# Kernel optimization log

Hardware: AMD Instinct MI355X
Metric: run time of the kernel (lower is better)

Reference implementation:

```python
import jax, jax.numpy as jnp
import numpy as np

D_MODEL = 1024
NUM_HEADS = 16
DEPTH = D_MODEL // NUM_HEADS
BATCH = 2
SEQ = 2048


def setup_inputs() -> dict:
    key = jax.random.key(0)
    ks = jax.random.split(key, 12)
    s = 1.0 / np.sqrt(D_MODEL)
    inp = {
        "v": jax.random.normal(ks[0], (BATCH, SEQ, D_MODEL), jnp.float32),
        "k": jax.random.normal(ks[1], (BATCH, SEQ, D_MODEL), jnp.float32),
        "q": jax.random.normal(ks[2], (BATCH, SEQ, D_MODEL), jnp.float32),
        # padding mask: 1 = masked, 0 = attend; float, broadcastable to (B,H,Sq,Sk)
        "mask": jax.random.randint(ks[3], (BATCH, 1, 1, SEQ), 0, 2).astype(jnp.float32),
        "training": 0,
        "wq_w": jax.random.normal(ks[4], (D_MODEL, D_MODEL), jnp.float32) * s,
        "wq_b": jnp.zeros((D_MODEL,), jnp.float32),
        "wk_w": jax.random.normal(ks[5], (D_MODEL, D_MODEL), jnp.float32) * s,
        "wk_b": jnp.zeros((D_MODEL,), jnp.float32),
        "wv_w": jax.random.normal(ks[6], (D_MODEL, D_MODEL), jnp.float32) * s,
        "wv_b": jnp.zeros((D_MODEL,), jnp.float32),
        "wo_w": jax.random.normal(ks[7], (D_MODEL, D_MODEL), jnp.float32) * s,
        "wo_b": jnp.zeros((D_MODEL,), jnp.float32),
    }
    return inp


def _split_heads(x, b):
    # (B, S, D) -> (B, H, S, depth)
    return x.reshape(b, -1, NUM_HEADS, DEPTH).transpose(0, 2, 1, 3)


def reference(v, k, q, mask, training, wq_w, wq_b, wk_w, wk_b, wv_w, wv_b, wo_w, wo_b):
    b = q.shape[0]
    qp = q @ wq_w + wq_b
    kp = k @ wk_w + wk_b
    vp = v @ wv_w + wv_b
    qh = _split_heads(qp, b)  # (B,H,Sq,depth)
    kh = _split_heads(kp, b)
    vh = _split_heads(vp, b)

    scale = 1.0 / jnp.sqrt(jnp.asarray(DEPTH, jnp.float32))
    logits = jnp.einsum("bhqd,bhkd->bhqk", qh, kh) * scale
    logits = logits + mask * (-1e9)
    attn = jax.nn.softmax(logits, axis=-1)                 # used for the value matmul
    out_h = jnp.einsum("bhqk,bhkd->bhqd", attn, vh)
    # NOTE: the original returns a second softmax over axis=2 (query axis)
    attn_weights = jax.nn.softmax(logits, axis=2)

    concat = out_h.transpose(0, 2, 1, 3).reshape(b, -1, D_MODEL)
    output = concat @ wo_w + wo_b
    return output, attn_weights
```

## Files before the change

kernel.cpp:

```cpp
#include <hip/hip_runtime.h>


typedef unsigned short u16;
typedef __attribute__((ext_vector_type(8))) short short8;
typedef __attribute__((ext_vector_type(8))) _Float16 half8;
typedef __attribute__((ext_vector_type(4))) float f32x4;

#define SEQ 2048
#define DMODEL 1024
#define NHEAD 16
#define DH 64

__device__ __forceinline__ u16 f2h(float f) {
  _Float16 h = (_Float16)f;
  return __builtin_bit_cast(u16, h);
}

__device__ __forceinline__ void gload16(const void* g, void* l) {
  __builtin_amdgcn_global_load_lds(
      (__attribute__((address_space(1))) void*)const_cast<void*>(g),
      (__attribute__((address_space(3))) void*)l, 16, 0, 0);
}

__global__ __launch_bounds__(256) void conv_qkv_k(
    const float* __restrict__ qs, const float* __restrict__ ks,
    const float* __restrict__ vs, u16* __restrict__ xq,
    u16* __restrict__ xk, u16* __restrict__ xv)
{
  int z = blockIdx.y;
  const float* s = (z == 0) ? qs : ((z == 1) ? ks : vs);
  u16* d = (z == 0) ? xq : ((z == 1) ? xk : xv);
  size_t i = ((size_t)blockIdx.x * 256 + threadIdx.x) * 8;
  float4 a = *(const float4*)(s + i);
  float4 b = *(const float4*)(s + i + 4);
  short8 o;
  o[0] = (short)f2h(a.x); o[1] = (short)f2h(a.y);
  o[2] = (short)f2h(a.z); o[3] = (short)f2h(a.w);
  o[4] = (short)f2h(b.x); o[5] = (short)f2h(b.y);
  o[6] = (short)f2h(b.z); o[7] = (short)f2h(b.w);
  *(short8*)(d + i) = o;
}

__global__ __launch_bounds__(256) void conv_wt_k(
    const float* __restrict__ w0, const float* __restrict__ w1,
    const float* __restrict__ w2, const float* __restrict__ w3,
    u16* __restrict__ t0, u16* __restrict__ t1,
    u16* __restrict__ t2, u16* __restrict__ t3)
{
  __shared__ u16 tile[64][65];
  int z = blockIdx.z;
  const float* W = (z==0)?w0:((z==1)?w1:((z==2)?w2:w3));
  u16* T = (z==0)?t0:((z==1)?t1:((z==2)?t2:t3));
  int k0 = blockIdx.x*64, n0 = blockIdx.y*64;
  int t = threadIdx.x;
  #pragma unroll
  for (int i=0;i<4;i++) {
    int idx = t + i*256;
    int r = idx >> 4, c4 = (idx & 15)*4;
    float4 f = *(const float4*)(W + (size_t)(k0+r)*DMODEL + n0 + c4);
    tile[r][c4+0] = f2h(f.x); tile[r][c4+1] = f2h(f.y);
    tile[r][c4+2] = f2h(f.z); tile[r][c4+3] = f2h(f.w);
  }
  __syncthreads();
  #pragma unroll
  for (int i=0;i<2;i++) {
    int idx = t + i*256;
    int nr = idx >> 3, c8 = (idx & 7)*8;
    short8 o;
    #pragma unroll
    for (int j=0;j<8;j++) o[j] = (short)tile[c8+j][nr];
    *(short8*)(T + (size_t)(n0+nr)*DMODEL + k0 + c8) = o;
  }
}

template<int EPI>
__global__ __launch_bounds__(256) void gemm16_k(
    const u16* __restrict__ A, const u16* __restrict__ Bt,
    const float* __restrict__ bias, void* __restrict__ outp)
{
  __shared__ u16 As[128*64];
  __shared__ u16 Bs[64*64];
  const int K = 1024;
  int tid = threadIdx.x, w = tid>>6, l = tid&63;
  int m0 = blockIdx.x*128, n0 = blockIdx.y*64;
  int wm = (w>>1)*64, wn = (w&1)*32;
  const f32x4 z4 = {0.f,0.f,0.f,0.f};
  f32x4 acc[4][2];
  #pragma unroll
  for (int mf=0;mf<4;mf++)
    #pragma unroll
    for (int nf=0;nf<2;nf++) acc[mf][nf] = z4;

  for (int k0=0;k0<K;k0+=64) {
    #pragma unroll
    for (int i=0;i<4;i++) {
      int cd = (w*4+i)*64 + l, r = cd>>3, p = cd&7, c = p ^ (r&7);
      gload16(A + (size_t)(m0+r)*K + k0 + c*8, (char*)As + (w*4+i)*1024);
    }
    #pragma unroll
    for (int i=0;i<2;i++) {
      int cd = (w*2+i)*64 + l, r = cd>>3, p = cd&7, c = p ^ (r&7);
      gload16(Bt + (size_t)(n0+r)*K + k0 + c*8, (char*)Bs + (w*2+i)*1024);
    }
    __syncthreads();
    half8 a[4][2], b[2][2];
    #pragma unroll
    for (int mf=0;mf<4;mf++)
      #pragma unroll
      for (int kf=0;kf<2;kf++) {
        int row = wm + mf*16 + (l&15);
        int ch = (kf*4 + (l>>4)) ^ (row&7);
        a[mf][kf] = *(const half8*)&As[row*64 + ch*8];
      }
    #pragma unroll
    for (int nf=0;nf<2;nf++)
      #pragma unroll
      for (int kf=0;kf<2;kf++) {
        int row = wn + nf*16 + (l&15);
        int ch = (kf*4 + (l>>4)) ^ (row&7);
        b[nf][kf] = *(const half8*)&Bs[row*64 + ch*8];
      }
    #pragma unroll
    for (int kf=0;kf<2;kf++)
      #pragma unroll
      for (int mf=0;mf<4;mf++)
        #pragma unroll
        for (int nf=0;nf<2;nf++)
          acc[mf][nf] = __builtin_amdgcn_mfma_f32_16x16x32_f16(
              a[mf][kf], b[nf][kf], acc[mf][nf], 0,0,0);
    __syncthreads();
  }
  #pragma unroll
  for (int mf=0;mf<4;mf++)
    #pragma unroll
    for (int nf=0;nf<2;nf++)
      #pragma unroll
      for (int r=0;r<4;r++) {
        int m = m0 + wm + mf*16 + (l>>4)*4 + r;
        int n = n0 + wn + nf*16 + (l&15);
        float v = acc[mf][nf][r] + bias[n];
        if (EPI == 0) {
          int bb = m >> 11, s = m & 2047, hh = n >> 6, dd = n & 63;
          ((u16*)outp)[((size_t)((bb*16+hh)*2048 + s))*64 + dd] = f2h(v);
        } else if (EPI == 1) {
          int bb = m >> 11, s = m & 2047, hh = n >> 6, dd = n & 63;
          ((u16*)outp)[((size_t)((bb*16+hh)*64 + dd))*2048 + s] = f2h(v);
        } else {
          ((float*)outp)[(size_t)m*DMODEL + n] = v;
        }
      }
}

__global__ __launch_bounds__(256) void flash_k(
    const u16* __restrict__ Qh, const u16* __restrict__ Kh,
    const u16* __restrict__ Vt, const float* __restrict__ mask,
    u16* __restrict__ Cc, float* __restrict__ colsum)
{
  __shared__ u16 Ks[2][64*64];
  __shared__ u16 Vs[2][64*64];
  __shared__ u16 Ps[4][16*64];
  __shared__ float colbuf[SEQ];
  int tid = threadIdx.x, w = tid>>6, l = tid&63;
  int lg = l>>4, li = l&15;
  int qb = blockIdx.x, bh = blockIdx.y, b = bh>>4, h = bh&15;
  const u16* Qb = Qh + (size_t)bh*SEQ*DH;
  const u16* Kb = Kh + (size_t)bh*SEQ*DH;
  const u16* Vb = Vt + (size_t)bh*DH*SEQ;
  const float* mrow = mask + (size_t)b*SEQ;
  for (int i=tid;i<SEQ;i+=256) colbuf[i] = 0.f;
  int q0 = qb*64 + w*16;
  half8 qf[2];
  #pragma unroll
  for (int kf=0;kf<2;kf++)
    qf[kf] = *(const half8*)&Qb[(size_t)(q0+li)*DH + kf*32 + lg*8];
  const f32x4 z4 = {0.f,0.f,0.f,0.f};
  f32x4 acc[4];
  float lrow[4];
  #pragma unroll
  for (int df=0;df<4;df++) acc[df] = z4;
  #pragma unroll
  for (int r=0;r<4;r++) lrow[r] = 0.f;
  u16* Pw = &Ps[w][0];

  auto stage = [&](int buf, int kt) {
    int k0 = kt*64;
    #pragma unroll
    for (int i=0;i<2;i++) {
      int cd = (w*2+i)*64 + l, r = cd>>3, p = cd&7, c = p ^ (r&7);
      gload16(Kb + (size_t)(k0+r)*DH + c*8, (char*)&Ks[buf][0] + (w*2+i)*1024);
    }
    #pragma unroll
    for (int i=0;i<2;i++) {
      int cd = (w*2+i)*64 + l, r = cd>>3, p = cd&7, c = p ^ (r&7);
      gload16(Vb + (size_t)r*SEQ + k0 + c*8, (char*)&Vs[buf][0] + (w*2+i)*1024);
    }
  };

  stage(0, 0);
  __syncthreads();

  for (int kt=0;kt<32;kt++) {
    int cur = kt & 1;
    if (kt < 31) stage(cur^1, kt+1);
    int k0 = kt*64;
    f32x4 s[4];
    #pragma unroll
    for (int nf=0;nf<4;nf++) s[nf] = z4;
    #pragma unroll
    for (int nf=0;nf<4;nf++) {
      int row = nf*16 + li;
      half8 kb0 = *(const half8*)&Ks[cur][row*64 + ((lg    ) ^ (row&7))*8];
      half8 kb1 = *(const half8*)&Ks[cur][row*64 + ((4 + lg) ^ (row&7))*8];
      s[nf] = __builtin_amdgcn_mfma_f32_16x16x32_f16(qf[0], kb0, s[nf],0,0,0);
      s[nf] = __builtin_amdgcn_mfma_f32_16x16x32_f16(qf[1], kb1, s[nf],0,0,0);
    }
    float mv[4], cp[4];
    #pragma unroll
    for (int nf=0;nf<4;nf++) {
      mv[nf] = mrow[k0 + nf*16 + li] * (-1e9f);
      cp[nf] = 0.f;
    }
    #pragma unroll
    for (int nf=0;nf<4;nf++) {
      f32x4 p;
      #pragma unroll
      for (int r=0;r<4;r++) {
        float e = __expf(s[nf][r]*0.125f + mv[nf]);
        e = fminf(e, 60000.f);
        p[r] = e;
        lrow[r] += e;
        cp[nf] += e;
      }
      s[nf] = p;
    }
    #pragma unroll
    for (int nf=0;nf<4;nf++) {
      float vsum = cp[nf];
      vsum += __shfl_xor(vsum, 16);
      vsum += __shfl_xor(vsum, 32);
      if (lg == 0) atomicAdd(&colbuf[k0 + nf*16 + li], vsum);
    }
    #pragma unroll
    for (int nf=0;nf<4;nf++) {
      int kc = nf*16 + li;
      #pragma unroll
      for (int r=0;r<4;r++) {
        int row = lg*4 + r;
        int ch = (kc>>3) ^ (row&7);
        Pw[row*64 + ch*8 + (kc&7)] = f2h(s[nf][r]);
      }
    }
    #pragma unroll
    for (int ks=0;ks<2;ks++) {
      half8 pa;
      {
        int row = li;
        int ch = (ks*4 + lg) ^ (row&7);
        pa = *(const half8*)&Pw[row*64 + ch*8];
      }
      #pragma unroll
      for (int df=0;df<4;df++) {
        int vrow = df*16 + li;
        half8 vb = *(const half8*)&Vs[cur][vrow*64 + ((ks*4 + lg) ^ (vrow&7))*8];
        acc[df] = __builtin_amdgcn_mfma_f32_16x16x32_f16(pa, vb, acc[df],0,0,0);
      }
    }
    __syncthreads();
  }
  #pragma unroll
  for (int r=0;r<4;r++) {
    float vsum = lrow[r];
    vsum += __shfl_xor(vsum, 1);
    vsum += __shfl_xor(vsum, 2);
    vsum += __shfl_xor(vsum, 4);
    vsum += __shfl_xor(vsum, 8);
    lrow[r] = 1.0f / vsum;
  }
  #pragma unroll
  for (int df=0;df<4;df++)
    #pragma unroll
    for (int r=0;r<4;r++) {
      int qrow = q0 + lg*4 + r;
      int col = h*64 + df*16 + li;
      Cc[(size_t)(b*SEQ + qrow)*DMODEL + col] = f2h(acc[df][r] * lrow[r]);
    }
  for (int i=tid;i<SEQ;i+=256) atomicAdd(&colsum[(size_t)bh*SEQ + i], colbuf[i]);
}

__global__ __launch_bounds__(256) void attnw_k(
    const u16* __restrict__ Qh, const u16* __restrict__ Kh,
    const float* __restrict__ mask, const float* __restrict__ colsum,
    float* __restrict__ outw)
{
  int tid = threadIdx.x, w = tid>>6, l = tid&63;
  int qb = blockIdx.x, bh = blockIdx.y, b = bh>>4;
  int kseg = blockIdx.z;
  const u16* Qb = Qh + (size_t)bh*SEQ*DH;
  const u16* Kb = Kh + (size_t)bh*SEQ*DH;
  const float* mrow = mask + (size_t)b*SEQ;
  const float* csrow = colsum + (size_t)bh*SEQ;
  float* obase = outw + (size_t)bh*SEQ*SEQ;
  int q0 = qb*128 + w*32;
  half8 qf[2][2];
  #pragma unroll
  for (int mf=0;mf<2;mf++)
    #pragma unroll
    for (int kf=0;kf<2;kf++)
      qf[mf][kf] = *(const half8*)&Qb[(size_t)(q0+mf*16+(l&15))*DH + kf*32 + (l>>4)*8];
  const f32x4 z4 = {0.f,0.f,0.f,0.f};
  for (int kt=kseg*2;kt<kseg*2+2;kt++) {
    int k0 = kt*128;
    f32x4 s[2][8];
    #pragma unroll
    for (int mf=0;mf<2;mf++)
      #pragma unroll
      for (int nf=0;nf<8;nf++) s[mf][nf] = z4;
    #pragma unroll
    for (int nf=0;nf<8;nf++) {
      const u16* kr = &Kb[(size_t)(k0+nf*16+(l&15))*DH + (l>>4)*8];
      half8 kb0 = *(const half8*)kr;
      half8 kb1 = *(const half8*)(kr + 32);
      #pragma unroll
      for (int mf=0;mf<2;mf++) {
        s[mf][nf] = __builtin_amdgcn_mfma_f32_16x16x32_f16(qf[mf][0], kb0, s[mf][nf],0,0,0);
        s[mf][nf] = __builtin_amdgcn_mfma_f32_16x16x32_f16(qf[mf][1], kb1, s[mf][nf],0,0,0);
      }
    }
    float rc[8];
    #pragma unroll
    for (int nf=0;nf<8;nf++) {
      int kk = k0 + nf*16 + (l&15);
      rc[nf] = (mrow[kk] != 0.f) ? -1.f : 1.0f/csrow[kk];
    }
    #pragma unroll
    for (int mf=0;mf<2;mf++)
      #pragma unroll
      for (int r=0;r<4;r++) {
        int q = q0 + mf*16 + (l>>4)*4 + r;
        float* rowp = obase + (size_t)q*SEQ + k0 + (l&15);
        #pragma unroll
        for (int nf=0;nf<8;nf++) {
          float val = (rc[nf] < 0.f) ? 4.8828125e-4f
                                     : __expf(s[mf][nf][r]*0.125f)*rc[nf];
          rowp[nf*16] = val;
        }
      }
  }
}

extern "C" void kernel_launch(void* const* d_in, const int* in_sizes, int n_in,
                              void* d_out, int out_size, void* d_ws, size_t ws_size,
                              hipStream_t stream) {
  (void)in_sizes; (void)n_in; (void)out_size; (void)ws_size;
  const float* v_in = (const float*)d_in[0];
  const float* k_in = (const float*)d_in[1];
  const float* q_in = (const float*)d_in[2];
  const float* mask = (const float*)d_in[3];
  const float* wq_w = (const float*)d_in[5];
  const float* wq_b = (const float*)d_in[6];
  const float* wk_w = (const float*)d_in[7];
  const float* wk_b = (const float*)d_in[8];
  const float* wv_w = (const float*)d_in[9];
  const float* wv_b = (const float*)d_in[10];
  const float* wo_w = (const float*)d_in[11];
  const float* wo_b = (const float*)d_in[12];

  char* ws = (char*)d_ws;
  const size_t MB = 1024*1024;
  u16* xq  = (u16*)(ws);
  u16* xk  = (u16*)(ws + 8*MB);
  u16* xv  = (u16*)(ws + 16*MB);
  u16* wqt = (u16*)(ws + 24*MB);
  u16* wkt = (u16*)(ws + 26*MB);
  u16* wvt = (u16*)(ws + 28*MB);
  u16* wot = (u16*)(ws + 30*MB);
  u16* qh  = (u16*)(ws + 32*MB);
  u16* kh  = (u16*)(ws + 40*MB);
  u16* vt  = (u16*)(ws + 48*MB);
  u16* cc  = (u16*)(ws + 56*MB);
  float* colsum = (float*)(ws + 64*MB);

  float* out0 = (float*)d_out;
  float* outw = out0 + (size_t)2*SEQ*DMODEL;

  (void)hipMemsetAsync(colsum, 0, (size_t)32*SEQ*sizeof(float), stream);
  conv_qkv_k<<<dim3(2048,3), 256, 0, stream>>>(q_in, k_in, v_in, xq, xk, xv);
  conv_wt_k<<<dim3(16,16,4), 256, 0, stream>>>(wq_w, wk_w, wv_w, wo_w, wqt, wkt, wvt, wot);
  gemm16_k<0><<<dim3(32,16), 256, 0, stream>>>(xq, wqt, wq_b, qh);
  gemm16_k<0><<<dim3(32,16), 256, 0, stream>>>(xk, wkt, wk_b, kh);
  gemm16_k<1><<<dim3(32,16), 256, 0, stream>>>(xv, wvt, wv_b, vt);
  flash_k<<<dim3(32,32), 256, 0, stream>>>(qh, kh, vt, mask, cc, colsum);
  attnw_k<<<dim3(16,32,8), 256, 0, stream>>>(qh, kh, mask, colsum, outw);
  gemm16_k<2><<<dim3(32,16), 256, 0, stream>>>(cc, wot, wo_b, out0);
}
```

Measured before the change: 429.1 us.

## Restage attention-weight stores through LDS and tighten flash loop barriers

The attention-weights kernel now transposes each wave's score tile through LDS so it can write full 16-byte vectors with nontemporal stores, replacing the scattered 4-byte row writes. The flash kernel issues the first K/V prefetch earlier and precomputes a mask flag array in shared memory. It also replaces the end-of-iteration __syncthreads with an explicit vmcnt wait plus raw s_barrier at the top of each iteration, so the next tile's loads overlap compute. This adds LDS usage and hand-written waitcnt logic, which is fragile if the load count per stage changes.

```diff
diff --git a/kernel.cpp b/kernel.cpp
--- a/kernel.cpp
+++ b/kernel.cpp
@@ -160,6 +160,7 @@
   __shared__ u16 Vs[2][64*64];
   __shared__ u16 Ps[4][16*64];
   __shared__ float colbuf[SEQ];
+  __shared__ u16 mflag[SEQ];
   int tid = threadIdx.x, w = tid>>6, l = tid&63;
   int lg = l>>4, li = l&15;
   int qb = blockIdx.x, bh = blockIdx.y, b = bh>>4, h = bh&15;
@@ -167,7 +168,26 @@
   const u16* Kb = Kh + (size_t)bh*SEQ*DH;
   const u16* Vb = Vt + (size_t)bh*DH*SEQ;
   const float* mrow = mask + (size_t)b*SEQ;
-  for (int i=tid;i<SEQ;i+=256) colbuf[i] = 0.f;
+
+  auto stage = [&](int buf, int kt) {
+    int k0 = kt*64;
+    #pragma unroll
+    for (int i=0;i<2;i++) {
+      int cd = (w*2+i)*64 + l, r = cd>>3, p = cd&7, c = p ^ (r&7);
+      gload16(Kb + (size_t)(k0+r)*DH + c*8, (char*)&Ks[buf][0] + (w*2+i)*1024);
+    }
+    #pragma unroll
+    for (int i=0;i<2;i++) {
+      int cd = (w*2+i)*64 + l, r = cd>>3, p = cd&7, c = p ^ (r&7);
+      gload16(Vb + (size_t)r*SEQ + k0 + c*8, (char*)&Vs[buf][0] + (w*2+i)*1024);
+    }
+  };
+
+  stage(0, 0);
+  for (int i=tid;i<SEQ;i+=256) {
+    colbuf[i] = 0.f;
+    mflag[i] = (mrow[i] != 0.f) ? 1 : 0;
+  }
   int q0 = qb*64 + w*16;
   half8 qf[2];
   #pragma unroll
@@ -181,28 +201,21 @@
   #pragma unroll
   for (int r=0;r<4;r++) lrow[r] = 0.f;
   u16* Pw = &Ps[w][0];
-
-  auto stage = [&](int buf, int kt) {
-    int k0 = kt*64;
-    #pragma unroll
-    for (int i=0;i<2;i++) {
-      int cd = (w*2+i)*64 + l, r = cd>>3, p = cd&7, c = p ^ (r&7);
-      gload16(Kb + (size_t)(k0+r)*DH + c*8, (char*)&Ks[buf][0] + (w*2+i)*1024);
-    }
-    #pragma unroll
-    for (int i=0;i<2;i++) {
-      int cd = (w*2+i)*64 + l, r = cd>>3, p = cd&7, c = p ^ (r&7);
-      gload16(Vb + (size_t)r*SEQ + k0 + c*8, (char*)&Vs[buf][0] + (w*2+i)*1024);
-    }
-  };
-
-  stage(0, 0);
   __syncthreads();
 
   for (int kt=0;kt<32;kt++) {
     int cur = kt & 1;
-    if (kt < 31) stage(cur^1, kt+1);
     int k0 = kt*64;
+    if (kt < 31) {
+      stage(cur^1, kt+1);
+      asm volatile("s_waitcnt vmcnt(4)" ::: "memory");
+    } else {
+      asm volatile("s_waitcnt vmcnt(0)" ::: "memory");
+    }
+    __builtin_amdgcn_sched_barrier(0);
+    __builtin_amdgcn_s_barrier();
+    __builtin_amdgcn_sched_barrier(0);
+
     f32x4 s[4];
     #pragma unroll
     for (int nf=0;nf<4;nf++) s[nf] = z4;
@@ -217,7 +230,7 @@
     float mv[4], cp[4];
     #pragma unroll
     for (int nf=0;nf<4;nf++) {
-      mv[nf] = mrow[k0 + nf*16 + li] * (-1e9f);
+      mv[nf] = mflag[k0 + nf*16 + li] ? -1e9f : 0.f;
       cp[nf] = 0.f;
     }
     #pragma unroll
@@ -265,8 +278,10 @@
         acc[df] = __builtin_amdgcn_mfma_f32_16x16x32_f16(pa, vb, acc[df],0,0,0);
       }
     }
-    __syncthreads();
-  }
+    __builtin_amdgcn_sched_barrier(0);
+    __builtin_amdgcn_s_barrier();
+  }
+  __syncthreads();
   #pragma unroll
   for (int r=0;r<4;r++) {
     float vsum = lrow[r];
@@ -292,7 +307,9 @@
     const float* __restrict__ mask, const float* __restrict__ colsum,
     float* __restrict__ outw)
 {
+  __shared__ float Ts[4][32*68];
   int tid = threadIdx.x, w = tid>>6, l = tid&63;
+  int lg = l>>4, li = l&15;
   int qb = blockIdx.x, bh = blockIdx.y, b = bh>>4;
   int kseg = blockIdx.z;
   const u16* Qb = Qh + (size_t)bh*SEQ*DH;
@@ -306,8 +323,10 @@
   for (int mf=0;mf<2;mf++)
     #pragma unroll
     for (int kf=0;kf<2;kf++)
-      qf[mf][kf] = *(const half8*)&Qb[(size_t)(q0+mf*16+(l&15))*DH + kf*32 + (l>>4)*8];
+      qf[mf][kf] = *(const half8*)&Qb[(size_t)(q0+mf*16+li)*DH + kf*32 + lg*8];
   const f32x4 z4 = {0.f,0.f,0.f,0.f};
+  const float UNIF = 4.8828125e-4f;
+  float* Tw = &Ts[w][0];
   for (int kt=kseg*2;kt<kseg*2+2;kt++) {
     int k0 = kt*128;
     f32x4 s[2][8];
@@ -317,7 +336,7 @@
       for (int nf=0;nf<8;nf++) s[mf][nf] = z4;
     #pragma unroll
     for (int nf=0;nf<8;nf++) {
-      const u16* kr = &Kb[(size_t)(k0+nf*16+(l&15))*DH + (l>>4)*8];
+      const u16* kr = &Kb[(size_t)(k0+nf*16+li)*DH + lg*8];
       half8 kb0 = *(const half8*)kr;
       half8 kb1 = *(const half8*)(kr + 32);
       #pragma unroll
@@ -329,22 +348,31 @@
     float rc[8];
     #pragma unroll
     for (int nf=0;nf<8;nf++) {
-      int kk = k0 + nf*16 + (l&15);
+      int kk = k0 + nf*16 + li;
       rc[nf] = (mrow[kk] != 0.f) ? -1.f : 1.0f/csrow[kk];
     }
     #pragma unroll
-    for (int mf=0;mf<2;mf++)
-      #pragma unroll
-      for (int r=0;r<4;r++) {
-        int q = q0 + mf*16 + (l>>4)*4 + r;
-        float* rowp = obase + (size_t)q*SEQ + k0 + (l&15);
+    for (int p=0;p<2;p++) {
+      #pragma unroll
+      for (int nf4=0;nf4<4;nf4++) {
+        int nf = 4*p + nf4;
         #pragma unroll
-        for (int nf=0;nf<8;nf++) {
-          float val = (rc[nf] < 0.f) ? 4.8828125e-4f
-                                     : __expf(s[mf][nf][r]*0.125f)*rc[nf];
-          rowp[nf*16] = val;
-        }
-      }
+        for (int mf=0;mf<2;mf++)
+          #pragma unroll
+          for (int r=0;r<4;r++) {
+            float val = (rc[nf] < 0.f) ? UNIF
+                                       : __expf(s[mf][nf][r]*0.125f)*rc[nf];
+            Tw[(mf*16 + lg*4 + r)*68 + nf4*16 + li] = val;
+          }
+      }
+      #pragma unroll
+      for (int r4=0;r4<8;r4++) {
+        int row = 4*r4 + lg;
+        f32x4 v = *(const f32x4*)&Tw[row*68 + 4*li];
+        __builtin_nontemporal_store(v,
+            (f32x4*)(obase + (size_t)(q0+row)*SEQ + k0 + 64*p + 4*li));
+      }
+    }
   }
 }
 
```

Result: faster. 391.4 us (-8.8%).
